# Optimization experiments

Measured on AMD Instinct MI355X. Metric: run time of the kernel, lower is better.

The kernel has to match this reference:

```python
import jax, jax.numpy as jnp
import numpy as np

N_NODES = 100000
N_EDGES = 1600000
D_IN = 128
D_HID = 128
D_OUT = 64


def _glorot(key, shape):
    lim = float(np.sqrt(6.0 / (shape[0] + shape[1])))
    return jax.random.uniform(key, shape, jnp.float32, -lim, lim)


def setup_inputs() -> dict:
    key = jax.random.key(0)
    ks = jax.random.split(key, 8)
    x = jax.random.normal(ks[0], (N_NODES, D_IN), jnp.float32)
    edge_index = jax.random.randint(ks[1], (2, N_EDGES), 0, N_NODES, jnp.int64)
    # SAGEConv layer 0: in=128 -> out=128 (lin_l with bias on aggregated, lin_r no bias on root)
    W_l0 = _glorot(ks[2], (D_IN, D_HID))
    b_l0 = jnp.zeros((D_HID,), jnp.float32)
    W_r0 = _glorot(ks[3], (D_IN, D_HID))
    # SAGEConv layer 1: in=128 -> out=64
    W_l1 = _glorot(ks[4], (D_HID, D_OUT))
    b_l1 = jnp.zeros((D_OUT,), jnp.float32)
    W_r1 = _glorot(ks[5], (D_HID, D_OUT))
    return {"x": x, "edge_index": edge_index,
            "W_l0": W_l0, "b_l0": b_l0, "W_r0": W_r0,
            "W_l1": W_l1, "b_l1": b_l1, "W_r1": W_r1}


def _sage_conv(x, src, dst, W_l, b_l, W_r):
    # mean aggregation of source features at targets (PyG SAGEConv default aggr='mean')
    msgs = x[src]                                              # [E, d_in] irregular gather
    agg = jax.ops.segment_sum(msgs, dst, num_segments=N_NODES)  # [N, d_in]
    cnt = jax.ops.segment_sum(jnp.ones((src.shape[0],), x.dtype), dst,
                              num_segments=N_NODES)            # [N]
    mean = agg / jnp.maximum(cnt, 1.0)[:, None]
    return mean @ W_l + b_l + x @ W_r


def reference(x, edge_index, W_l0, b_l0, W_r0, W_l1, b_l1, W_r1):
    src, dst = edge_index[0], edge_index[1]
    h = _sage_conv(x, src, dst, W_l0, b_l0, W_r0)
    h = jax.nn.relu(h)
    # dropout is identity at inference (training=False)
    out = _sage_conv(h, src, dst, W_l1, b_l1, W_r1)
    return out
```

## Files before the change

### kernel.cpp

```cpp
#include <hip/hip_runtime.h>
#include <type_traits>

#define NN 100000
#define NE 1600000
#define DF 128
#define NBKT 196
#define BKT_SHIFT 9
#define EPB 6250

typedef unsigned short ushort_t;
typedef unsigned int uint_t;
typedef __bf16 bf16x8 __attribute__((ext_vector_type(8)));
typedef float f32x4 __attribute__((ext_vector_type(4)));

union ABFrag { uint4 u; bf16x8 v; ushort_t s[8]; };

__device__ __forceinline__ ushort_t f2bf(float f) {
    uint_t u;
    __builtin_memcpy(&u, &f, 4);
    uint_t rounding = 0x7FFFu + ((u >> 16) & 1u);
    u += rounding;
    return (ushort_t)(u >> 16);
}
__device__ __forceinline__ float lo_f(uint_t u) { return __uint_as_float(u << 16); }
__device__ __forceinline__ float hi_f(uint_t u) { return __uint_as_float(u & 0xffff0000u); }
__device__ __forceinline__ uint_t pack2(float a, float b) {
    return (uint_t)f2bf(a) | ((uint_t)f2bf(b) << 16);
}

__device__ __forceinline__ int detect64(const int* ei, int* s64) {
    if (threadIdx.x < 64) {
        int v = ei[threadIdx.x];
        bool ok = ((threadIdx.x & 1) == 0) || (v == 0);
        unsigned long long m = __ballot(ok);
        if (threadIdx.x == 0) *s64 = (m == 0xFFFFFFFFFFFFFFFFULL) ? 1 : 0;
    }
    __syncthreads();
    return *s64;
}

__global__ __launch_bounds__(256) void k_bktcnt(const int* __restrict__ ei,
                                                int* __restrict__ M) {
    __shared__ int cnt[NBKT];
    __shared__ int s64;
    int t = threadIdx.x, blk = blockIdx.x;
    int is64 = detect64(ei, &s64);
    for (int i = t; i < NBKT; i += 256) cnt[i] = 0;
    __syncthreads();
    int e0 = blk * EPB;
    if (is64) {
        const long long* p = (const long long*)ei;
        for (int i = t; i < EPB; i += 256) {
            int d = (int)p[(size_t)NE + e0 + i];
            atomicAdd(&cnt[d >> BKT_SHIFT], 1);
        }
    } else {
        for (int i = t; i < EPB; i += 256) {
            int d = ei[NE + e0 + i];
            atomicAdd(&cnt[d >> BKT_SHIFT], 1);
        }
    }
    __syncthreads();
    for (int i = t; i < NBKT; i += 256) M[i * 256 + blk] = cnt[i];
}

__global__ __launch_bounds__(256) void k_colscan(int* __restrict__ M, int* __restrict__ colsum) {
    __shared__ int sm[256];
    int t = threadIdx.x, b = blockIdx.x;
    int v = M[b * 256 + t];
    sm[t] = v;
    __syncthreads();
    for (int o = 1; o < 256; o <<= 1) {
        int add = (t >= o) ? sm[t - o] : 0;
        __syncthreads();
        sm[t] += add;
        __syncthreads();
    }
    M[b * 256 + t] = sm[t] - v;
    if (t == 255) colsum[b] = sm[255];
}

__global__ __launch_bounds__(256) void k_bktscan(const int* __restrict__ colsum,
                                                 int* __restrict__ bkbase, int* __restrict__ rs) {
    __shared__ int sm[256];
    int t = threadIdx.x;
    int v = (t < NBKT) ? colsum[t] : 0;
    sm[t] = v;
    __syncthreads();
    for (int o = 1; o < 256; o <<= 1) {
        int add = (t >= o) ? sm[t - o] : 0;
        __syncthreads();
        sm[t] += add;
        __syncthreads();
    }
    if (t <= NBKT) bkbase[t] = sm[t] - v;
    if (t == 0) rs[NN] = NE;
}

__global__ __launch_bounds__(256) void k_bktscatter(const int* __restrict__ ei,
                                                    const int* __restrict__ M,
                                                    const int* __restrict__ bkbase,
                                                    uint2* __restrict__ tmp) {
    __shared__ int cur[NBKT];
    __shared__ int s64;
    int t = threadIdx.x, blk = blockIdx.x;
    int is64 = detect64(ei, &s64);
    for (int i = t; i < NBKT; i += 256) cur[i] = bkbase[i] + M[i * 256 + blk];
    __syncthreads();
    int e0 = blk * EPB;
    if (is64) {
        const long long* p = (const long long*)ei;
        for (int i = t; i < EPB; i += 256) {
            int e = e0 + i;
            int s = (int)p[e], d = (int)p[(size_t)NE + e];
            int pos = atomicAdd(&cur[d >> BKT_SHIFT], 1);
            tmp[pos] = make_uint2((uint_t)s, (uint_t)d);
        }
    } else {
        for (int i = t; i < EPB; i += 256) {
            int e = e0 + i;
            int s = ei[e], d = ei[NE + e];
            int pos = atomicAdd(&cur[d >> BKT_SHIFT], 1);
            tmp[pos] = make_uint2((uint_t)s, (uint_t)d);
        }
    }
}

__global__ __launch_bounds__(256) void k_bktsort(const uint2* __restrict__ tmp,
                                                 const int* __restrict__ bkbase,
                                                 int* __restrict__ rs, int* __restrict__ esrc) {
    __shared__ int hist[512];
    __shared__ int curp[512];
    int t = threadIdx.x, b = blockIdx.x;
    int nbase = b << BKT_SHIFT;
    int bb = bkbase[b], be = bkbase[b + 1];
    hist[t] = 0;
    hist[t + 256] = 0;
    __syncthreads();
    for (int i = bb + t; i < be; i += 256)
        atomicAdd(&hist[(int)tmp[i].y - nbase], 1);
    __syncthreads();
    int ov0 = hist[t], ov1 = hist[t + 256];
    for (int o = 1; o < 512; o <<= 1) {
        int v0 = (t >= o) ? hist[t - o] : 0;
        int v1 = (t + 256 >= o) ? hist[t + 256 - o] : 0;
        __syncthreads();
        hist[t] += v0;
        hist[t + 256] += v1;
        __syncthreads();
    }
    int ex0 = bb + hist[t] - ov0;
    int ex1 = bb + hist[t + 256] - ov1;
    int n0 = nbase + t, n1 = nbase + t + 256;
    if (n0 < NN) rs[n0] = ex0;
    if (n1 < NN) rs[n1] = ex1;
    curp[t] = ex0;
    curp[t + 256] = ex1;
    __syncthreads();
    for (int i = bb + t; i < be; i += 256) {
        uint2 pr = tmp[i];
        int pos = atomicAdd(&curp[(int)pr.y - nbase], 1);
        esrc[pos] = (int)pr.x;
    }
}

#define CAST_B 12501
__global__ void k_prep(const float* __restrict__ x, ushort_t* __restrict__ xb,
                       const float* __restrict__ Wl0, const float* __restrict__ Wr0,
                       ushort_t* __restrict__ pw0,
                       const float* __restrict__ Wl1, const float* __restrict__ Wr1,
                       ushort_t* __restrict__ pw1) {
    const int n4 = NN * DF / 4;
    int blk = blockIdx.x, t = threadIdx.x;
    if (blk < CAST_B) {
        int i = blk * 256 + t;
        if (i < n4) {
            float4 f = ((const float4*)x)[i];
            uint2 o;
            o.x = pack2(f.x, f.y);
            o.y = pack2(f.z, f.w);
            ((uint2*)xb)[i] = o;
        } else if (i < n4 + 32) {
            ((uint2*)xb)[i] = make_uint2(0u, 0u);
        }
    } else if (blk < CAST_B + 128) {
        int idx = (blk - CAST_B) * 256 + t;
        int j = idx & 7;
        int lane = (idx >> 3) & 63;
        int rem = idx / 512;
        int tt = rem % 8;
        int s = rem / 8;
        int quad = lane >> 4, l16 = lane & 15;
        int k = (s & 3) * 32 + quad * 8 + j;
        int n = tt * 16 + l16;
        const float* W = (s < 4) ? Wl0 : Wr0;
        pw0[idx] = f2bf(W[k * 128 + n]);
    } else {
        int idx = (blk - CAST_B - 128) * 256 + t;
        int j = idx & 7;
        int lane = (idx >> 3) & 63;
        int rem = idx / 512;
        int tt = rem % 8;
        int s = rem / 8;
        int quad = lane >> 4, l16 = lane & 15;
        int k = s * 32 + quad * 8 + j;
        int n = (tt & 3) * 16 + l16;
        const float* W = (tt < 4) ? Wl1 : Wr1;
        pw1[idx] = f2bf(W[k * 64 + n]);
    }
}

__global__ __launch_bounds__(256) void k_fused(const ushort_t* __restrict__ xb,
                                               const int* __restrict__ rs,
                                               const int* __restrict__ esrc,
                                               const ushort_t* __restrict__ pw0,
                                               const float* __restrict__ bl0,
                                               const ushort_t* __restrict__ pw1,
                                               const float* __restrict__ bl1,
                                               ushort_t* __restrict__ tbuf,
                                               float* __restrict__ rbuf) {
    __shared__ ushort_t m_lds[16][136];
    __shared__ ushort_t h_lds[16][136];
    int tid = threadIdx.x;
    int wv = tid >> 6, lane = tid & 63;
    int l16 = lane & 15, quad = lane >> 4, gbase = lane & 48;
    int n0 = blockIdx.x * 16;

    int n = n0 + wv * 4 + quad;
    int s0 = rs[n];
    int deg = rs[n + 1] - s0;
    int md = deg;
    md = max(md, __shfl_xor(md, 16));
    md = max(md, __shfl_xor(md, 32));
    float acc[8] = {0.f, 0.f, 0.f, 0.f, 0.f, 0.f, 0.f, 0.f};
    const ushort_t* fb = xb + l16 * 8;
    int clampIdx = (deg > 0) ? deg - 1 : 0;
    for (int c = 0; c < md; c += 16) {
        int ii = c + l16;
        if (ii > clampIdx) ii = clampIdx;
        int my = esrc[s0 + ii];
        uint4 v[16];
#pragma unroll
        for (int e = 0; e < 16; e++) {
            int r = __shfl(my, gbase + e);
            r = (c + e < deg) ? r : NN;
            v[e] = *(const uint4*)(fb + (size_t)r * DF);
        }
#pragma unroll
        for (int e = 0; e < 16; e++) {
            acc[0] += lo_f(v[e].x); acc[1] += hi_f(v[e].x);
            acc[2] += lo_f(v[e].y); acc[3] += hi_f(v[e].y);
            acc[4] += lo_f(v[e].z); acc[5] += hi_f(v[e].z);
            acc[6] += lo_f(v[e].w); acc[7] += hi_f(v[e].w);
        }
    }
    {
        float inv = 1.0f / (float)(deg > 0 ? deg : 1);
        int nl = wv * 4 + quad;
        uint_t* mp = (uint_t*)&m_lds[nl][l16 * 8];
        mp[0] = pack2(acc[0] * inv, acc[1] * inv);
        mp[1] = pack2(acc[2] * inv, acc[3] * inv);
        mp[2] = pack2(acc[4] * inv, acc[5] * inv);
        mp[3] = pack2(acc[6] * inv, acc[7] * inv);
    }
    __syncthreads();

    const int kofs = quad * 8;
    f32x4 c0[2] = {(f32x4){0.f, 0.f, 0.f, 0.f}, (f32x4){0.f, 0.f, 0.f, 0.f}};
#pragma unroll
    for (int s = 0; s < 8; s++) {
        ABFrag a;
        if (s < 4)
            a.u = *(const uint4*)&m_lds[l16][(s & 3) * 32 + kofs];
        else
            a.u = *(const uint4*)(xb + (size_t)(n0 + l16) * DF + (s & 3) * 32 + kofs);
#pragma unroll
        for (int i = 0; i < 2; i++) {
            int t = wv * 2 + i;
            ABFrag b;
            b.u = *(const uint4*)(pw0 + ((size_t)(s * 8 + t) * 64 + lane) * 8);
            c0[i] = __builtin_amdgcn_mfma_f32_16x16x32_bf16(a.v, b.v, c0[i], 0, 0, 0);
        }
    }
#pragma unroll
    for (int i = 0; i < 2; i++) {
        int col = wv * 32 + i * 16 + l16;
        float bv = bl0[col];
#pragma unroll
        for (int r = 0; r < 4; r++) {
            float v = fmaxf(c0[i][r] + bv, 0.f);
            h_lds[quad * 4 + r][col] = f2bf(v);
        }
    }
    __syncthreads();

    f32x4 c1[2] = {(f32x4){0.f, 0.f, 0.f, 0.f}, (f32x4){0.f, 0.f, 0.f, 0.f}};
#pragma unroll
    for (int s = 0; s < 4; s++) {
        ABFrag a;
        a.u = *(const uint4*)&h_lds[l16][s * 32 + kofs];
#pragma unroll
        for (int i = 0; i < 2; i++) {
            int t = wv * 2 + i;
            ABFrag b;
            b.u = *(const uint4*)(pw1 + ((size_t)(s * 8 + t) * 64 + lane) * 8);
            c1[i] = __builtin_amdgcn_mfma_f32_16x16x32_bf16(a.v, b.v, c1[i], 0, 0, 0);
        }
    }
#pragma unroll
    for (int i = 0; i < 2; i++) {
        int t = wv * 2 + i;
        int cc = (t & 3) * 16 + l16;
        if (t < 4) {
#pragma unroll
            for (int r = 0; r < 4; r++)
                tbuf[(size_t)(n0 + quad * 4 + r) * 64 + cc] = f2bf(c1[i][r]);
        } else {
            float bv = bl1[cc];
#pragma unroll
            for (int r = 0; r < 4; r++)
                rbuf[(size_t)(n0 + quad * 4 + r) * 64 + cc] = c1[i][r] + bv;
        }
    }
    if (blockIdx.x == 0 && tid < 32)
        ((uint_t*)(tbuf + (size_t)NN * 64))[tid] = 0u;
}

__global__ __launch_bounds__(256) void k_agg2(const ushort_t* __restrict__ tbuf,
                                              const float* __restrict__ rbuf,
                                              const int* __restrict__ rs,
                                              const int* __restrict__ esrc,
                                              float* __restrict__ out) {
    int wv = threadIdx.x >> 6;
    int lane = threadIdx.x & 63;
    int li = lane & 7;
    int gbase = lane & 56;
    int n = (blockIdx.x * 4 + wv) * 8 + (lane >> 3);
    int s0 = rs[n];
    int deg = rs[n + 1] - s0;
    int md = deg;
    md = max(md, __shfl_xor(md, 8));
    md = max(md, __shfl_xor(md, 16));
    md = max(md, __shfl_xor(md, 32));
    float acc[8] = {0.f, 0.f, 0.f, 0.f, 0.f, 0.f, 0.f, 0.f};
    const ushort_t* fb = tbuf + li * 8;
    int clampIdx = (deg > 0) ? deg - 1 : 0;
    for (int c = 0; c < md; c += 8) {
        int ii = c + li;
        if (ii > clampIdx) ii = clampIdx;
        int my = esrc[s0 + ii];
        uint4 v[8];
#pragma unroll
        for (int e = 0; e < 8; e++) {
            int r = __shfl(my, gbase + e);
            r = (c + e < deg) ? r : NN;
            v[e] = *(const uint4*)(fb + (size_t)r * 64);
        }
#pragma unroll
        for (int e = 0; e < 8; e++) {
            acc[0] += lo_f(v[e].x); acc[1] += hi_f(v[e].x);
            acc[2] += lo_f(v[e].y); acc[3] += hi_f(v[e].y);
            acc[4] += lo_f(v[e].z); acc[5] += hi_f(v[e].z);
            acc[6] += lo_f(v[e].w); acc[7] += hi_f(v[e].w);
        }
    }
    float inv = 1.0f / (float)(deg > 0 ? deg : 1);
    const float4* rp = (const float4*)(rbuf + (size_t)n * 64 + li * 8);
    float4 ra = rp[0], rb = rp[1];
    float4 oa, ob;
    oa.x = acc[0] * inv + ra.x; oa.y = acc[1] * inv + ra.y;
    oa.z = acc[2] * inv + ra.z; oa.w = acc[3] * inv + ra.w;
    ob.x = acc[4] * inv + rb.x; ob.y = acc[5] * inv + rb.y;
    ob.z = acc[6] * inv + rb.z; ob.w = acc[7] * inv + rb.w;
    float4* op = (float4*)(out + (size_t)n * 64 + li * 8);
    op[0] = oa;
    op[1] = ob;
}

extern "C" void kernel_launch(void* const* d_in, const int* in_sizes, int n_in,
                              void* d_out, int out_size, void* d_ws, size_t ws_size,
                              hipStream_t stream) {
    const float* x   = (const float*)d_in[0];
    const int*   ei  = (const int*)d_in[1];
    const float* Wl0 = (const float*)d_in[2];
    const float* bl0 = (const float*)d_in[3];
    const float* Wr0 = (const float*)d_in[4];
    const float* Wl1 = (const float*)d_in[5];
    const float* bl1 = (const float*)d_in[6];
    const float* Wr1 = (const float*)d_in[7];
    float* out = (float*)d_out;

    char* ws = (char*)d_ws;
    size_t off = 0;
    auto alloc = [&](size_t b) {
        size_t o = off;
        off += (b + 255) & ~(size_t)255;
        return o;
    };
    int* rs     = (int*)(ws + alloc((size_t)(NN + 1) * 4));
    int* M      = (int*)(ws + alloc((size_t)NBKT * 256 * 4));
    int* colsum = (int*)(ws + alloc((size_t)NBKT * 4));
    int* bkbase = (int*)(ws + alloc((size_t)(NBKT + 1) * 4));
    int* esrc   = (int*)(ws + alloc((size_t)NE * 4));
    ushort_t* pw0  = (ushort_t*)(ws + alloc((size_t)8 * 8 * 512 * 2));
    ushort_t* pw1  = (ushort_t*)(ws + alloc((size_t)4 * 8 * 512 * 2));
    ushort_t* xb   = (ushort_t*)(ws + alloc((size_t)(NN + 1) * DF * 2));
    ushort_t* tbuf = (ushort_t*)(ws + alloc((size_t)(NN + 1) * 64 * 2));
    float*    rbuf = (float*)(ws + alloc((size_t)NN * 64 * 4));
    uint2* tmp = (uint2*)rbuf;

    k_bktcnt<<<256, 256, 0, stream>>>(ei, M);
    k_colscan<<<NBKT, 256, 0, stream>>>(M, colsum);
    k_bktscan<<<1, 256, 0, stream>>>(colsum, bkbase, rs);
    k_bktscatter<<<256, 256, 0, stream>>>(ei, M, bkbase, tmp);
    k_bktsort<<<NBKT, 256, 0, stream>>>(tmp, bkbase, rs, esrc);
    k_prep<<<CAST_B + 128 + 64, 256, 0, stream>>>(x, xb, Wl0, Wr0, pw0, Wl1, Wr1, pw1);
    k_fused<<<NN / 16, 256, 0, stream>>>(xb, rs, esrc, pw0, bl0, pw1, bl1, tbuf, rbuf);
    k_agg2<<<NN / 32, 256, 0, stream>>>(tbuf, rbuf, rs, esrc, out);
}
```

Measured before the change: 290.3 us.

## Sort nodes by degree for balanced aggregation and split fused kernel into agg and GEMMs

Adds a counting sort of nodes by in-degree (capped at 511) to build a permutation, so the aggregation kernels process nodes with similar degree within a wavefront and lose less work to max-degree divergence. The previous fused aggregate+GEMM+GEMM kernel is split into a standalone layer-0 aggregation writing bf16 means, a 64-row-block GEMM producing the ReLU hidden layer, and a second GEMM producing tbuf/rbuf. This costs four extra small launches plus two extra 25 MB intermediate round trips through memory, and the permuted node order makes output writes scattered.

```diff
diff --git a/kernel.cpp b/kernel.cpp
--- a/kernel.cpp
+++ b/kernel.cpp
@@ -7,6 +7,7 @@
 #define NBKT 196
 #define BKT_SHIFT 9
 #define EPB 6250
+#define NPB2 391
 
 typedef unsigned short ushort_t;
 typedef unsigned int uint_t;
@@ -95,6 +96,21 @@
     }
     if (t <= NBKT) bkbase[t] = sm[t] - v;
     if (t == 0) rs[NN] = NE;
+}
+
+__global__ void k_scan512(const int* __restrict__ c2, int* __restrict__ dbase) {
+    __shared__ int sm[512];
+    int t = threadIdx.x;
+    int v = c2[t];
+    sm[t] = v;
+    __syncthreads();
+    for (int o = 1; o < 512; o <<= 1) {
+        int add = (t >= o) ? sm[t - o] : 0;
+        __syncthreads();
+        sm[t] += add;
+        __syncthreads();
+    }
+    dbase[t] = sm[t] - v;
 }
 
 __global__ __launch_bounds__(256) void k_bktscatter(const int* __restrict__ ei,
@@ -161,6 +177,47 @@
         uint2 pr = tmp[i];
         int pos = atomicAdd(&curp[(int)pr.y - nbase], 1);
         esrc[pos] = (int)pr.x;
+    }
+}
+
+__global__ __launch_bounds__(256) void k_dcnt(const int* __restrict__ rs, int* __restrict__ M2) {
+    __shared__ int cnt[512];
+    int t = threadIdx.x, b = blockIdx.x;
+    cnt[t] = 0;
+    cnt[t + 256] = 0;
+    __syncthreads();
+    int base = b * NPB2;
+    for (int i = t; i < NPB2; i += 256) {
+        int n = base + i;
+        if (n < NN) {
+            int d = rs[n + 1] - rs[n];
+            if (d > 511) d = 511;
+            atomicAdd(&cnt[d], 1);
+        }
+    }
+    __syncthreads();
+    M2[t * 256 + b] = cnt[t];
+    M2[(t + 256) * 256 + b] = cnt[t + 256];
+}
+
+__global__ __launch_bounds__(256) void k_dperm(const int* __restrict__ rs,
+                                               const int* __restrict__ M2,
+                                               const int* __restrict__ dbase,
+                                               int* __restrict__ perm) {
+    __shared__ int cur[512];
+    int t = threadIdx.x, b = blockIdx.x;
+    cur[t] = dbase[t] + M2[t * 256 + b];
+    cur[t + 256] = dbase[t + 256] + M2[(t + 256) * 256 + b];
+    __syncthreads();
+    int base = b * NPB2;
+    for (int i = t; i < NPB2; i += 256) {
+        int n = base + i;
+        if (n < NN) {
+            int d = rs[n + 1] - rs[n];
+            if (d > 511) d = 511;
+            int pos = atomicAdd(&cur[d], 1);
+            perm[pos] = n;
+        }
     }
 }
 
@@ -210,25 +267,19 @@
     }
 }
 
-__global__ __launch_bounds__(256) void k_fused(const ushort_t* __restrict__ xb,
-                                               const int* __restrict__ rs,
-                                               const int* __restrict__ esrc,
-                                               const ushort_t* __restrict__ pw0,
-                                               const float* __restrict__ bl0,
-                                               const ushort_t* __restrict__ pw1,
-                                               const float* __restrict__ bl1,
-                                               ushort_t* __restrict__ tbuf,
-                                               float* __restrict__ rbuf) {
-    __shared__ ushort_t m_lds[16][136];
-    __shared__ ushort_t h_lds[16][136];
-    int tid = threadIdx.x;
-    int wv = tid >> 6, lane = tid & 63;
+__global__ __launch_bounds__(256) void k_agg0(const ushort_t* __restrict__ xb,
+                                              const int* __restrict__ rs,
+                                              const int* __restrict__ esrc,
+                                              const int* __restrict__ perm,
+                                              ushort_t* __restrict__ outm) {
+    int wv = threadIdx.x >> 6;
+    int lane = threadIdx.x & 63;
     int l16 = lane & 15, quad = lane >> 4, gbase = lane & 48;
-    int n0 = blockIdx.x * 16;
-
-    int n = n0 + wv * 4 + quad;
+    int slot = (blockIdx.x * 4 + wv) * 4 + quad;
+    int n = perm[slot];
     int s0 = rs[n];
     int deg = rs[n + 1] - s0;
+    if (deg == 0) s0 = 0;
     int md = deg;
     md = max(md, __shfl_xor(md, 16));
     md = max(md, __shfl_xor(md, 32));
@@ -254,90 +305,132 @@
             acc[6] += lo_f(v[e].w); acc[7] += hi_f(v[e].w);
         }
     }
-    {
-        float inv = 1.0f / (float)(deg > 0 ? deg : 1);
-        int nl = wv * 4 + quad;
-        uint_t* mp = (uint_t*)&m_lds[nl][l16 * 8];
-        mp[0] = pack2(acc[0] * inv, acc[1] * inv);
-        mp[1] = pack2(acc[2] * inv, acc[3] * inv);
-        mp[2] = pack2(acc[4] * inv, acc[5] * inv);
-        mp[3] = pack2(acc[6] * inv, acc[7] * inv);
-    }
-    __syncthreads();
-
+    float inv = 1.0f / (float)(deg > 0 ? deg : 1);
+    uint4 o;
+    o.x = pack2(acc[0] * inv, acc[1] * inv);
+    o.y = pack2(acc[2] * inv, acc[3] * inv);
+    o.z = pack2(acc[4] * inv, acc[5] * inv);
+    o.w = pack2(acc[6] * inv, acc[7] * inv);
+    *(uint4*)(outm + (size_t)n * DF + l16 * 8) = o;
+}
+
+__global__ __launch_bounds__(256) void k_gemm0(const ushort_t* __restrict__ A0,
+                                               const ushort_t* __restrict__ A1,
+                                               const ushort_t* __restrict__ Wpk,
+                                               const float* __restrict__ bias,
+                                               ushort_t* __restrict__ out) {
+    int warp = threadIdx.x >> 6;
+    int lane = threadIdx.x & 63;
+    int quad = lane >> 4;
+    int l16 = lane & 15;
+    int m0 = blockIdx.x * 64 + warp * 16;
+
+    int rowA = m0 + l16;
+    if (rowA >= NN) rowA = NN - 1;
     const int kofs = quad * 8;
-    f32x4 c0[2] = {(f32x4){0.f, 0.f, 0.f, 0.f}, (f32x4){0.f, 0.f, 0.f, 0.f}};
+
+    f32x4 acc[8];
+#pragma unroll
+    for (int t = 0; t < 8; t++) acc[t] = (f32x4){0.f, 0.f, 0.f, 0.f};
+
 #pragma unroll
     for (int s = 0; s < 8; s++) {
+        const ushort_t* Ab = (s < 4) ? A0 : A1;
+        int kk = (s & 3) * 32 + kofs;
         ABFrag a;
-        if (s < 4)
-            a.u = *(const uint4*)&m_lds[l16][(s & 3) * 32 + kofs];
-        else
-            a.u = *(const uint4*)(xb + (size_t)(n0 + l16) * DF + (s & 3) * 32 + kofs);
-#pragma unroll
-        for (int i = 0; i < 2; i++) {
-            int t = wv * 2 + i;
+        a.u = *(const uint4*)(Ab + (size_t)rowA * DF + kk);
+#pragma unroll
+        for (int t = 0; t < 8; t++) {
             ABFrag b;
-            b.u = *(const uint4*)(pw0 + ((size_t)(s * 8 + t) * 64 + lane) * 8);
-            c0[i] = __builtin_amdgcn_mfma_f32_16x16x32_bf16(a.v, b.v, c0[i], 0, 0, 0);
-        }
-    }
-#pragma unroll
-    for (int i = 0; i < 2; i++) {
-        int col = wv * 32 + i * 16 + l16;
-        float bv = bl0[col];
+            b.u = *(const uint4*)(Wpk + ((size_t)(s * 8 + t) * 64 + lane) * 8);
+            acc[t] = __builtin_amdgcn_mfma_f32_16x16x32_bf16(a.v, b.v, acc[t], 0, 0, 0);
+        }
+    }
+
+#pragma unroll
+    for (int t = 0; t < 8; t++) {
+        int col = t * 16 + l16;
+        float bv = bias[col];
 #pragma unroll
         for (int r = 0; r < 4; r++) {
-            float v = fmaxf(c0[i][r] + bv, 0.f);
-            h_lds[quad * 4 + r][col] = f2bf(v);
-        }
-    }
-    __syncthreads();
-
-    f32x4 c1[2] = {(f32x4){0.f, 0.f, 0.f, 0.f}, (f32x4){0.f, 0.f, 0.f, 0.f}};
+            int row = m0 + quad * 4 + r;
+            if (row < NN) {
+                float v = fmaxf(acc[t][r] + bv, 0.f);
+                out[(size_t)row * DF + col] = f2bf(v);
+            }
+        }
+    }
+}
+
+__global__ __launch_bounds__(256) void k_gemm2(const ushort_t* __restrict__ A,
+                                               const ushort_t* __restrict__ Wpk,
+                                               const float* __restrict__ bias,
+                                               ushort_t* __restrict__ tbuf,
+                                               float* __restrict__ rbuf) {
+    int warp = threadIdx.x >> 6;
+    int lane = threadIdx.x & 63;
+    int quad = lane >> 4;
+    int l16 = lane & 15;
+    int m0 = blockIdx.x * 64 + warp * 16;
+
+    int rowA = m0 + l16;
+    if (rowA >= NN) rowA = NN - 1;
+    const int kofs = quad * 8;
+
+    f32x4 acc[8];
+#pragma unroll
+    for (int t = 0; t < 8; t++) acc[t] = (f32x4){0.f, 0.f, 0.f, 0.f};
+
 #pragma unroll
     for (int s = 0; s < 4; s++) {
+        int kk = s * 32 + kofs;
         ABFrag a;
-        a.u = *(const uint4*)&h_lds[l16][s * 32 + kofs];
-#pragma unroll
-        for (int i = 0; i < 2; i++) {
-            int t = wv * 2 + i;
+        a.u = *(const uint4*)(A + (size_t)rowA * DF + kk);
+#pragma unroll
+        for (int t = 0; t < 8; t++) {
             ABFrag b;
-            b.u = *(const uint4*)(pw1 + ((size_t)(s * 8 + t) * 64 + lane) * 8);
-            c1[i] = __builtin_amdgcn_mfma_f32_16x16x32_bf16(a.v, b.v, c1[i], 0, 0, 0);
-        }
-    }
-#pragma unroll
-    for (int i = 0; i < 2; i++) {
-        int t = wv * 2 + i;
+            b.u = *(const uint4*)(Wpk + ((size_t)(s * 8 + t) * 64 + lane) * 8);
+            acc[t] = __builtin_amdgcn_mfma_f32_16x16x32_bf16(a.v, b.v, acc[t], 0, 0, 0);
+        }
+    }
+
+#pragma unroll
+    for (int t = 0; t < 8; t++) {
         int cc = (t & 3) * 16 + l16;
         if (t < 4) {
 #pragma unroll
-            for (int r = 0; r < 4; r++)
-                tbuf[(size_t)(n0 + quad * 4 + r) * 64 + cc] = f2bf(c1[i][r]);
+            for (int r = 0; r < 4; r++) {
+                int row = m0 + quad * 4 + r;
+                if (row < NN) tbuf[(size_t)row * 64 + cc] = f2bf(acc[t][r]);
+            }
         } else {
-            float bv = bl1[cc];
-#pragma unroll
-            for (int r = 0; r < 4; r++)
-                rbuf[(size_t)(n0 + quad * 4 + r) * 64 + cc] = c1[i][r] + bv;
-        }
-    }
-    if (blockIdx.x == 0 && tid < 32)
-        ((uint_t*)(tbuf + (size_t)NN * 64))[tid] = 0u;
+            float bv = bias[cc];
+#pragma unroll
+            for (int r = 0; r < 4; r++) {
+                int row = m0 + quad * 4 + r;
+                if (row < NN) rbuf[(size_t)row * 64 + cc] = acc[t][r] + bv;
+            }
+        }
+    }
+    if (blockIdx.x == 0 && threadIdx.x < 32)
+        ((uint_t*)(tbuf + (size_t)NN * 64))[threadIdx.x] = 0u;
 }
 
 __global__ __launch_bounds__(256) void k_agg2(const ushort_t* __restrict__ tbuf,
                                               const float* __restrict__ rbuf,
                                               const int* __restrict__ rs,
                                               const int* __restrict__ esrc,
+                                              const int* __restrict__ perm,
                                               float* __restrict__ out) {
     int wv = threadIdx.x >> 6;
     int lane = threadIdx.x & 63;
     int li = lane & 7;
     int gbase = lane & 56;
-    int n = (blockIdx.x * 4 + wv) * 8 + (lane >> 3);
+    int slot = (blockIdx.x * 4 + wv) * 8 + (lane >> 3);
+    int n = perm[slot];
     int s0 = rs[n];
     int deg = rs[n + 1] - s0;
+    if (deg == 0) s0 = 0;
     int md = deg;
     md = max(md, __shfl_xor(md, 8));
     md = max(md, __shfl_xor(md, 16));
@@ -397,24 +490,37 @@
         off += (b + 255) & ~(size_t)255;
         return o;
     };
-    int* rs     = (int*)(ws + alloc((size_t)(NN + 1) * 4));
-    int* M      = (int*)(ws + alloc((size_t)NBKT * 256 * 4));
-    int* colsum = (int*)(ws + alloc((size_t)NBKT * 4));
-    int* bkbase = (int*)(ws + alloc((size_t)(NBKT + 1) * 4));
-    int* esrc   = (int*)(ws + alloc((size_t)NE * 4));
+    int* rs      = (int*)(ws + alloc((size_t)(NN + 1) * 4));
+    int* M       = (int*)(ws + alloc((size_t)NBKT * 256 * 4));
+    int* colsum  = (int*)(ws + alloc((size_t)NBKT * 4));
+    int* bkbase  = (int*)(ws + alloc((size_t)(NBKT + 1) * 4));
+    int* M2      = (int*)(ws + alloc((size_t)512 * 256 * 4));
+    int* colsum2 = (int*)(ws + alloc((size_t)512 * 4));
+    int* dbase   = (int*)(ws + alloc((size_t)512 * 4));
+    int* perm    = (int*)(ws + alloc((size_t)NN * 4));
+    int* esrc    = (int*)(ws + alloc((size_t)NE * 4));
     ushort_t* pw0  = (ushort_t*)(ws + alloc((size_t)8 * 8 * 512 * 2));
     ushort_t* pw1  = (ushort_t*)(ws + alloc((size_t)4 * 8 * 512 * 2));
     ushort_t* xb   = (ushort_t*)(ws + alloc((size_t)(NN + 1) * DF * 2));
+    ushort_t* mean = (ushort_t*)(ws + alloc((size_t)NN * DF * 2));
+    ushort_t* h    = (ushort_t*)(ws + alloc((size_t)NN * DF * 2));
     ushort_t* tbuf = (ushort_t*)(ws + alloc((size_t)(NN + 1) * 64 * 2));
-    float*    rbuf = (float*)(ws + alloc((size_t)NN * 64 * 4));
-    uint2* tmp = (uint2*)rbuf;
+    uint2* tmp = (uint2*)mean;
+    float* rbuf = (float*)mean;
 
     k_bktcnt<<<256, 256, 0, stream>>>(ei, M);
     k_colscan<<<NBKT, 256, 0, stream>>>(M, colsum);
     k_bktscan<<<1, 256, 0, stream>>>(colsum, bkbase, rs);
     k_bktscatter<<<256, 256, 0, stream>>>(ei, M, bkbase, tmp);
     k_bktsort<<<NBKT, 256, 0, stream>>>(tmp, bkbase, rs, esrc);
+    k_dcnt<<<256, 256, 0, stream>>>(rs, M2);
+    k_colscan<<<512, 256, 0, stream>>>(M2, colsum2);
+    k_scan512<<<1, 512, 0, stream>>>(colsum2, dbase);
+    k_dperm<<<256, 256, 0, stream>>>(rs, M2, dbase, perm);
     k_prep<<<CAST_B + 128 + 64, 256, 0, stream>>>(x, xb, Wl0, Wr0, pw0, Wl1, Wr1, pw1);
-    k_fused<<<NN / 16, 256, 0, stream>>>(xb, rs, esrc, pw0, bl0, pw1, bl1, tbuf, rbuf);
-    k_agg2<<<NN / 32, 256, 0, stream>>>(tbuf, rbuf, rs, esrc, out);
-}
+
+    k_agg0<<<NN / 16, 256, 0, stream>>>(xb, rs, esrc, perm, mean);
+    k_gemm0<<<(NN + 63) / 64, 256, 0, stream>>>(mean, xb, pw0, bl0, h);
+    k_gemm2<<<(NN + 63) / 64, 256, 0, stream>>>(h, pw1, bl1, tbuf, rbuf);
+    k_agg2<<<NN / 32, 256, 0, stream>>>(tbuf, rbuf, rs, esrc, perm, out);
+}
```

After: 339.0 us. 16.8% more time.
